# Kernel tuning notes

Measured on AMD Instinct MI355X. Metric: run time of the kernel, lower is better.

## Reference

```python
import jax, jax.numpy as jnp
import numpy as np
from jax import lax

DROP_PROB = 0.1
BLOCK_SIZE = 7
B, C, H, W = 64, 256, 56, 56
HM, WM = H - (BLOCK_SIZE - 1), W - (BLOCK_SIZE - 1)


def setup_inputs() -> dict:
    key = jax.random.key(0)
    k1, k2 = jax.random.split(key)
    x = jax.random.normal(k1, (B, C, H, W), dtype=jnp.float32)
    mask_u = jax.random.uniform(k2, (B, C, HM, WM), dtype=jnp.float32)
    return {"x": x, "mask_u": mask_u}


def reference(x, mask_u):
    bs = BLOCK_SIZE
    feat = x.shape[2]
    # gamma as in _compute_gamma
    gamma = DROP_PROB / bs**2 * feat**2 / (feat - bs + 1) ** 2
    # Bernoulli(gamma) sample, deterministic given mask_u
    mask = (mask_u < gamma).astype(x.dtype)  # (B,C,HM,WM)
    # The nonzero/scatter block expansion in the original is exactly a
    # stride-1 max-pool with a bs x bs window and (bs-1, bs-1) zero padding,
    # producing the (B,C,H,W) padded dropped-region mask.
    blocked = lax.reduce_window(
        mask, 0.0, lax.max,
        window_dimensions=(1, 1, bs, bs),
        window_strides=(1, 1, 1, 1),
        padding=((0, 0), (0, 0), (bs - 1, bs - 1), (bs - 1, bs - 1)),
    )
    block_mask = 1.0 - blocked  # (B,C,H,W)
    scale = block_mask.size / block_mask.sum()
    return x * block_mask * scale
```

## Files before the change

kernel.cpp:

```cpp
#include <hip/hip_runtime.h>


#define BB 64
#define CC 256
#define HH 56
#define WW 56
#define HMM 50
#define WMM 50
#define BS 7

static constexpr unsigned int NPLANE = BB * CC;
static constexpr unsigned int NTOT   = BB * CC * HH * WW;
static constexpr unsigned int NV     = NTOT / 4;
static constexpr unsigned int NP     = NV / 2;
static constexpr unsigned int PLANEF = HMM * WMM;
static constexpr unsigned int PLANE4 = PLANEF / 4;

typedef float f32x4 __attribute__((ext_vector_type(4)));

__global__ void __launch_bounds__(256) dropblock_mask_kernel(
    const float* __restrict__ mask_u,
    unsigned long long* __restrict__ rowmask,
    unsigned int* __restrict__ plane_cnt,
    float gamma)
{
    const unsigned int tid   = threadIdx.x;
    const unsigned int wid   = tid >> 6;
    const unsigned int lane  = tid & 63u;
    const unsigned int plane = blockIdx.x * 4u + wid;

    __shared__ float4 lds4[4 * PLANE4];
    const float* lds = reinterpret_cast<const float*>(lds4);

    {
        const float4* src = reinterpret_cast<const float4*>(mask_u)
                          + (size_t)blockIdx.x * (4 * PLANE4);
        #pragma unroll
        for (unsigned int r = 0; r < 10; ++r) {
            unsigned int idx = tid + r * 256u;
            if (idx < 4 * PLANE4) lds4[idx] = src[idx];
        }
    }
    __syncthreads();

    const float* mu = lds + wid * PLANEF;
    unsigned long long my_d = 0ull;

    #pragma unroll
    for (int i = 0; i < HMM; ++i) {
        float v = (lane < WMM) ? mu[i * WMM + lane] : 1.0f;
        unsigned long long m = __ballot(v < gamma);
        unsigned long long d = m | (m << 1);
        d |= d << 2;
        d |= d << 3;
        if (lane == (unsigned)i) my_d = d;
    }

    unsigned long long blocked = my_d;
    blocked |= __shfl_up(blocked, 1, 64);
    blocked |= __shfl_up(blocked, 2, 64);
    blocked |= __shfl_up(blocked, 3, 64);

    if (lane < HH) rowmask[plane * HH + lane] = blocked;

    unsigned int cnt = __popcll(blocked);
    #pragma unroll
    for (int off = 32; off > 0; off >>= 1)
        cnt += __shfl_down(cnt, off, 64);
    if (lane == 0) plane_cnt[plane] = cnt;
}

__global__ void __launch_bounds__(1024) dropblock_scale_kernel(
    const unsigned int* __restrict__ plane_cnt,
    float* __restrict__ scale_out)
{
    __shared__ unsigned int ssum[16];
    const unsigned int t = threadIdx.x;

    const uint4* pc4 = reinterpret_cast<const uint4*>(plane_cnt);
    uint4 a = pc4[t];
    uint4 b = pc4[t + 1024];
    uint4 c = pc4[t + 2048];
    uint4 d = pc4[t + 3072];
    unsigned int s = a.x + a.y + a.z + a.w
                   + b.x + b.y + b.z + b.w
                   + c.x + c.y + c.z + c.w
                   + d.x + d.y + d.z + d.w;

    #pragma unroll
    for (int off = 32; off > 0; off >>= 1)
        s += __shfl_down(s, off, 64);
    if ((t & 63u) == 0u) ssum[t >> 6] = s;
    __syncthreads();

    if (t < 16) {
        unsigned int v = ssum[t];
        #pragma unroll
        for (int off = 8; off > 0; off >>= 1)
            v += __shfl_down(v, off, 64);
        if (t == 0) {
            *scale_out = (float)NTOT / (float)(NTOT - v);
        }
    }
}

__global__ void __launch_bounds__(256) dropblock_apply_kernel(
    const float* __restrict__ x,
    const unsigned long long* __restrict__ rowmask,
    const float* __restrict__ scale_ptr,
    float* __restrict__ out)
{
    const unsigned int p = blockIdx.x * 256u + threadIdx.x;
    const float scale = *scale_ptr;

    unsigned int plane = p / 392u;
    unsigned int rem   = p - plane * 392u;
    unsigned int row   = rem / 7u;
    unsigned int pc    = rem - row * 7u;

    unsigned int rbits =
        (unsigned int)(rowmask[plane * HH + row] >> (pc * 8u)) & 0xffu;

    const f32x4* xp = reinterpret_cast<const f32x4*>(x) + (size_t)p * 2u;
    f32x4 a = xp[0];
    f32x4 b = xp[1];

    f32x4 oa, ob;
    #pragma unroll
    for (int j = 0; j < 4; ++j)
        oa[j] = ((rbits >> j) & 1u) ? 0.0f : a[j] * scale;
    #pragma unroll
    for (int j = 0; j < 4; ++j)
        ob[j] = ((rbits >> (4 + j)) & 1u) ? 0.0f : b[j] * scale;

    f32x4* op = reinterpret_cast<f32x4*>(out) + (size_t)p * 2u;
    op[0] = oa;
    op[1] = ob;
}

extern "C" void kernel_launch(void* const* d_in, const int* in_sizes, int n_in,
                              void* d_out, int out_size, void* d_ws, size_t ws_size,
                              hipStream_t stream) {
    const float* x      = (const float*)d_in[0];
    const float* mask_u = (const float*)d_in[1];
    float* out          = (float*)d_out;

    float* scale_ws             = (float*)d_ws;
    unsigned int* plane_cnt     = (unsigned int*)((char*)d_ws + 64);
    unsigned long long* rowmask = (unsigned long long*)((char*)d_ws + 65600);

    const double gd = 0.1 / ((double)BS * BS) * ((double)HH * HH) /
                      (((double)HH - BS + 1.0) * ((double)HH - BS + 1.0));
    const float gamma = (float)gd;

    dropblock_mask_kernel<<<NPLANE / 4, 256, 0, stream>>>(
        mask_u, rowmask, plane_cnt, gamma);

    dropblock_scale_kernel<<<1, 1024, 0, stream>>>(plane_cnt, scale_ws);

    dropblock_apply_kernel<<<NP / 256u, 256, 0, stream>>>(
        x, rowmask, scale_ws, out);
}
```

Baseline: 438.4 us.

## Use persistent grid in apply kernel with row masks staged in LDS

The apply kernel now launches 1024 blocks, and each block handles 16 whole planes instead of one thread per 8 floats across about 50k blocks. Each block first copies its planes' row masks into shared memory, then loops over float4 elements, reading mask bits from LDS. This is meant to cut block launch and scheduling overhead and the redundant global row-mask loads. In exchange it adds a block barrier and per-iteration integer divides, and the fixed grid gives less parallelism slack on a bandwidth-bound pass.

After: 447.4 us. +2.1%, slower.

```diff
diff --git a/kernel.cpp b/kernel.cpp
--- a/kernel.cpp
+++ b/kernel.cpp
@@ -12,9 +12,13 @@
 static constexpr unsigned int NPLANE = BB * CC;
 static constexpr unsigned int NTOT   = BB * CC * HH * WW;
 static constexpr unsigned int NV     = NTOT / 4;
-static constexpr unsigned int NP     = NV / 2;
 static constexpr unsigned int PLANEF = HMM * WMM;
 static constexpr unsigned int PLANE4 = PLANEF / 4;
+static constexpr unsigned int AGRID  = 1024;
+static constexpr unsigned int PPB    = NPLANE / AGRID;
+static constexpr unsigned int F4PP   = HH * WW / 4;
+static constexpr unsigned int F4PB   = PPB * F4PP;
+static constexpr unsigned int KITER  = F4PB / 256;
 
 typedef float f32x4 __attribute__((ext_vector_type(4)));
 
@@ -110,32 +114,39 @@
     const float* __restrict__ scale_ptr,
     float* __restrict__ out)
 {
-    const unsigned int p = blockIdx.x * 256u + threadIdx.x;
+    const unsigned int tid = threadIdx.x;
+    const unsigned int b   = blockIdx.x;
+
+    __shared__ unsigned long long rsh[PPB * HH];
+
+    const unsigned long long* rsrc = rowmask + (size_t)b * (PPB * HH);
+    #pragma unroll
+    for (unsigned int r = 0; r < 4; ++r) {
+        unsigned int i = tid + r * 256u;
+        if (i < PPB * HH) rsh[i] = rsrc[i];
+    }
     const float scale = *scale_ptr;
+    __syncthreads();
 
-    unsigned int plane = p / 392u;
-    unsigned int rem   = p - plane * 392u;
-    unsigned int row   = rem / 7u;
-    unsigned int pc    = rem - row * 7u;
+    const f32x4* xp = reinterpret_cast<const f32x4*>(x)  + (size_t)b * F4PB;
+    f32x4*       op = reinterpret_cast<f32x4*>(out)      + (size_t)b * F4PB;
 
-    unsigned int rbits =
-        (unsigned int)(rowmask[plane * HH + row] >> (pc * 8u)) & 0xffu;
+    #pragma unroll 7
+    for (unsigned int k = 0; k < KITER; ++k) {
+        unsigned int il  = tid + k * 256u;
+        unsigned int pl  = il / F4PP;
+        unsigned int rem = il - pl * F4PP;
+        unsigned int row = rem / 14u;
+        unsigned int col = (rem - row * 14u) * 4u;
 
-    const f32x4* xp = reinterpret_cast<const f32x4*>(x) + (size_t)p * 2u;
-    f32x4 a = xp[0];
-    f32x4 b = xp[1];
-
-    f32x4 oa, ob;
-    #pragma unroll
-    for (int j = 0; j < 4; ++j)
-        oa[j] = ((rbits >> j) & 1u) ? 0.0f : a[j] * scale;
-    #pragma unroll
-    for (int j = 0; j < 4; ++j)
-        ob[j] = ((rbits >> (4 + j)) & 1u) ? 0.0f : b[j] * scale;
-
-    f32x4* op = reinterpret_cast<f32x4*>(out) + (size_t)p * 2u;
-    op[0] = oa;
-    op[1] = ob;
+        unsigned long long rm = rsh[pl * HH + row];
+        f32x4 xv = xp[il];
+        f32x4 o;
+        #pragma unroll
+        for (int j = 0; j < 4; ++j)
+            o[j] = ((rm >> (col + j)) & 1ull) ? 0.0f : xv[j] * scale;
+        op[il] = o;
+    }
 }
 
 extern "C" void kernel_launch(void* const* d_in, const int* in_sizes, int n_in,
@@ -158,6 +169,6 @@
 
     dropblock_scale_kernel<<<1, 1024, 0, stream>>>(plane_cnt, scale_ws);
 
-    dropblock_apply_kernel<<<NP / 256u, 256, 0, stream>>>(
+    dropblock_apply_kernel<<<AGRID, 256, 0, stream>>>(
         x, rowmask, scale_ws, out);
 }
```
